# Kernel optimization log

Hardware: AMD Instinct MI355X
Metric: run time of the kernel (lower is better)

The kernel has to match this reference:

```python
import jax, jax.numpy as jnp
import numpy as np

N = 50_000       # nodes
E = 1_600_000    # edges per edge set (avg degree 32)
D = 128          # hidden dim
F_IN = 1273      # fixed num_features in NetGIN
G = 512          # graphs in batch
STEPS = 6        # Set2Set processing steps
BN_EPS = 1e-5


def setup_inputs() -> dict:
    key = jax.random.key(0)
    ks = iter(jax.random.split(key, 40))
    def rn(shape, fan_in):
        return jax.random.normal(next(ks), shape, jnp.float32) / np.float32(np.sqrt(fan_in))
    inp = {}
    inp["x"] = jax.random.normal(next(ks), (N, F_IN), jnp.float32)
    for i in (1, 2, 3):
        inp[f"edge_index_{i}"] = jax.random.randint(next(ks), (2, E), 0, N, jnp.int32)
    inp["batch"] = jnp.sort(jax.random.randint(next(ks), (N,), 0, G, jnp.int32))
    # GINConv MLPs: layer 1 has input F_IN, layers 2-6 have input D
    inp["conv1_W1"] = rn((3, F_IN, D), F_IN)
    inp["conv1_b1"] = jnp.zeros((3, D), jnp.float32)
    inp["conv_rest_W1"] = rn((5, 3, D, D), D)
    inp["conv_rest_b1"] = jnp.zeros((5, 3, D), jnp.float32)
    inp["conv_W2"] = rn((6, 3, D, D), D)
    inp["conv_b2"] = jnp.zeros((6, 3, D), jnp.float32)
    inp["conv_bn1_g"] = jnp.ones((6, 3, D), jnp.float32)
    inp["conv_bn1_b"] = jnp.zeros((6, 3, D), jnp.float32)
    inp["conv_bn2_g"] = jnp.ones((6, 3, D), jnp.float32)
    inp["conv_bn2_b"] = jnp.zeros((6, 3, D), jnp.float32)
    inp["conv_eps"] = jnp.zeros((6, 3), jnp.float32)  # train_eps=True, init 0
    # fusion MLPs (3*D -> D -> D)
    inp["mlp_W1"] = rn((6, 3 * D, D), 3 * D)
    inp["mlp_b1"] = jnp.zeros((6, D), jnp.float32)
    inp["mlp_bn1_g"] = jnp.ones((6, D), jnp.float32)
    inp["mlp_bn1_b"] = jnp.zeros((6, D), jnp.float32)
    inp["mlp_W2"] = rn((6, D, D), D)
    inp["mlp_b2"] = jnp.zeros((6, D), jnp.float32)
    inp["mlp_bn2_g"] = jnp.ones((6, D), jnp.float32)
    inp["mlp_bn2_b"] = jnp.zeros((6, D), jnp.float32)
    # Set2Set single-layer LSTM: input 2D, hidden D; gate order i,f,g,o
    inp["lstm_Wih"] = rn((4 * D, 2 * D), 2 * D)
    inp["lstm_Whh"] = rn((4 * D, D), D)
    inp["lstm_bih"] = jnp.zeros((4 * D,), jnp.float32)
    inp["lstm_bhh"] = jnp.zeros((4 * D,), jnp.float32)
    inp["fc1_W"] = rn((2 * D, D), 2 * D)
    inp["fc1_b"] = jnp.zeros((D,), jnp.float32)
    inp["fc4_W"] = rn((D, 12), D)
    inp["fc4_b"] = jnp.zeros((12,), jnp.float32)
    return inp


def _bn(x, g, b):
    # BatchNorm1d in training mode: batch statistics (biased var), eps=1e-5
    mu = jnp.mean(x, axis=0)
    var = jnp.var(x, axis=0)
    return g * (x - mu) * jax.lax.rsqrt(var + BN_EPS) + b


def _mlp2(h, W1, b1, g1, bb1, W2, b2, g2, bb2):
    h = jax.nn.relu(_bn(h @ W1 + b1, g1, bb1))
    return jax.nn.relu(_bn(h @ W2 + b2, g2, bb2))


def _gin(h, ei, eps, W1, b1, g1, bb1, W2, b2, g2, bb2):
    # sum-aggregate neighbor features: out[dst] += h[src]
    agg = jax.ops.segment_sum(h[ei[0]], ei[1], num_segments=h.shape[0])
    return _mlp2((1.0 + eps) * h + agg, W1, b1, g1, bb1, W2, b2, g2, bb2)


def _forward(x, conv1_W1, conv1_b1, conv_rest_W1, conv_rest_b1, conv_W2, conv_b2,
             conv_bn1_g, conv_bn1_b, conv_bn2_g, conv_bn2_b, conv_eps,
             mlp_W1, mlp_b1, mlp_bn1_g, mlp_bn1_b, mlp_W2, mlp_b2, mlp_bn2_g, mlp_bn2_b,
             lstm_Wih, lstm_Whh, lstm_bih, lstm_bhh, fc1_W, fc1_b, fc4_W, fc4_b,
             edge_index_1, edge_index_2, edge_index_3, batch):
    edges = (edge_index_1, edge_index_2, edge_index_3)
    h = x
    for l in range(6):
        xs = []
        for k in range(3):
            W1 = conv1_W1[k] if l == 0 else conv_rest_W1[l - 1, k]
            b1 = conv1_b1[k] if l == 0 else conv_rest_b1[l - 1, k]
            xk = jax.nn.relu(_gin(h, edges[k], conv_eps[l, k], W1, b1,
                                  conv_bn1_g[l, k], conv_bn1_b[l, k],
                                  conv_W2[l, k], conv_b2[l, k],
                                  conv_bn2_g[l, k], conv_bn2_b[l, k]))
            xs.append(xk)
        h = _mlp2(jnp.concatenate(xs, axis=-1),
                  mlp_W1[l], mlp_b1[l], mlp_bn1_g[l], mlp_bn1_b[l],
                  mlp_W2[l], mlp_b2[l], mlp_bn2_g[l], mlp_bn2_b[l])
    # Set2Set readout (processing_steps=6)
    q_star = jnp.zeros((G, 2 * D), h.dtype)
    hh = jnp.zeros((G, D), h.dtype)
    cc = jnp.zeros((G, D), h.dtype)
    for _ in range(STEPS):
        gates = q_star @ lstm_Wih.T + hh @ lstm_Whh.T + lstm_bih + lstm_bhh
        i_g, f_g, g_g, o_g = jnp.split(gates, 4, axis=-1)
        cc = jax.nn.sigmoid(f_g) * cc + jax.nn.sigmoid(i_g) * jnp.tanh(g_g)
        hh = jax.nn.sigmoid(o_g) * jnp.tanh(cc)
        q = hh
        e = jnp.sum(h * q[batch], axis=-1)              # [N]
        emax = jax.ops.segment_max(e, batch, num_segments=G)
        ex = jnp.exp(e - emax[batch])
        denom = jax.ops.segment_sum(ex, batch, num_segments=G)
        a = ex / denom[batch]                            # per-graph softmax
        r = jax.ops.segment_sum(a[:, None] * h, batch, num_segments=G)
        q_star = jnp.concatenate([q, r], axis=-1)
    out = jax.nn.relu(q_star @ fc1_W + fc1_b)
    return out @ fc4_W + fc4_b                           # [G, 12]


def reference(x, conv1_W1, conv1_b1, conv_rest_W1, conv_rest_b1, conv_W2, conv_b2,
              conv_bn1_g, conv_bn1_b, conv_bn2_g, conv_bn2_b, conv_eps,
              mlp_W1, mlp_b1, mlp_bn1_g, mlp_bn1_b, mlp_W2, mlp_b2, mlp_bn2_g, mlp_bn2_b,
              lstm_Wih, lstm_Whh, lstm_bih, lstm_bhh, fc1_W, fc1_b, fc4_W, fc4_b,
              edge_index_1, edge_index_2, edge_index_3, batch):
    return _forward(x, conv1_W1, conv1_b1, conv_rest_W1, conv_rest_b1, conv_W2, conv_b2,
                    conv_bn1_g, conv_bn1_b, conv_bn2_g, conv_bn2_b, conv_eps,
                    mlp_W1, mlp_b1, mlp_bn1_g, mlp_bn1_b, mlp_W2, mlp_b2, mlp_bn2_g, mlp_bn2_b,
                    lstm_Wih, lstm_Whh, lstm_bih, lstm_bhh, fc1_W, fc1_b, fc4_W, fc4_b,
                    edge_index_1, edge_index_2, edge_index_3, batch)
```

## Files before the change

kernel.cpp:

```cpp
#include <hip/hip_runtime.h>
#include <cstdint>
#include <cstddef>

#define NN 50000
#define EE 1600000
#define GG 512
#define FIN 1273

typedef unsigned short u16;
typedef unsigned int u32;
typedef __attribute__((ext_vector_type(8))) short short8;
typedef __attribute__((ext_vector_type(4))) float f32x4;

__device__ __forceinline__ float sigmf(float x) { return 1.f / (1.f + expf(-x)); }

__device__ __forceinline__ void splitbf(float v, u16& hi, u16& lo) {
    const u32 u = __float_as_uint(v);
    hi = (u16)(u >> 16);
    const float rem = v - __uint_as_float(u & 0xffff0000u);
    lo = (u16)(__float_as_uint(rem) >> 16);
}

__device__ __forceinline__ void gload_lds16(const void* g, void* l) {
    __builtin_amdgcn_global_load_lds(
        (const __attribute__((address_space(1))) void*)g,
        (__attribute__((address_space(3))) void*)l, 16, 0, 0);
}

template <int MODE>
__global__ __launch_bounds__(256) void gemm_bn(
    const float* __restrict__ A, size_t strideA, int lda, int K, int Kreal,
    const float* __restrict__ st, int stSlice, int stMat,
    const float* __restrict__ ga, const float* __restrict__ be,
    int gbSlice, int gbMat,
    const u16* __restrict__ Bhi, const u16* __restrict__ Blo, size_t strideB,
    const float* __restrict__ bias, int biasMat,
    float* __restrict__ C, int ldc, int coffStep,
    int M, int do_stats, float* __restrict__ stats_out, int ostatMat)
{
    __shared__ u16 lsAhi[128 * 64];
    __shared__ u16 lsAlo[128 * 64];
    __shared__ u16 lsBhi[128 * 64];
    __shared__ u16 lsBlo[128 * 64];
    const int tid = threadIdx.x;
    const int wave = tid >> 6, lane = tid & 63;
    const int mat = blockIdx.x;
    const int row0 = blockIdx.y * 128;
    const int coff = mat * coffStep;
    A += (size_t)mat * strideA;
    if (MODE == 1) {
        st += mat * stMat; ga += mat * gbMat; be += mat * gbMat;
    }
    if (bias) bias += mat * biasMat;
    if (do_stats) stats_out += mat * ostatMat;
    const u16* Bh = Bhi + (size_t)mat * strideB;
    const u16* Bl = Blo + (size_t)mat * strideB;
    const int wm = wave >> 1, wn = wave & 1;
    f32x4 acc[4][4] = {};

    for (int k0 = 0; k0 < K; k0 += 64) {
        if (k0) __syncthreads();
        float scv[8], shv[8];
        if (MODE == 1) {
            const int kb = k0 + (tid & 7) * 8;
            const int s = kb >> 7, d0 = kb & 127;
            const float* stS = st + s * stSlice;
            const float* gS  = ga + s * gbSlice;
            const float* beS = be + s * gbSlice;
            #pragma unroll
            for (int e = 0; e < 8; ++e) {
                const int d = d0 + e;
                const float mu = stS[d] * (1.f / NN);
                const float var = fmaxf(stS[128 + d] * (1.f / NN) - mu * mu, 0.f);
                const float sc = gS[d] * rsqrtf(var + 1e-5f);
                scv[e] = sc;
                shv[e] = beS[d] - sc * mu;
            }
        }
        #pragma unroll
        for (int i = 0; i < 4; ++i) {
            const int slot = i * 256 + tid;
            const int r = slot >> 3, ch = tid & 7;
            int gr = row0 + r; if (gr >= M) gr = M - 1;
            const int kb = k0 + ch * 8;
            u16 th[8], tl[8];
            if (MODE == 0) {
                const float* src = A + (size_t)gr * lda + kb;
                if (kb + 8 <= Kreal) {
                    const float4 v0 = *(const float4*)(src);
                    const float4 v1 = *(const float4*)(src + 4);
                    const float va[8] = {v0.x, v0.y, v0.z, v0.w,
                                         v1.x, v1.y, v1.z, v1.w};
                    #pragma unroll
                    for (int e = 0; e < 8; ++e) splitbf(va[e], th[e], tl[e]);
                } else {
                    #pragma unroll
                    for (int e = 0; e < 8; ++e) {
                        const float v = (kb + e < Kreal) ? src[e] : 0.f;
                        splitbf(v, th[e], tl[e]);
                    }
                }
            } else {
                const float* src = A + (size_t)gr * lda + kb;
                const float4 v0 = *(const float4*)(src);
                const float4 v1 = *(const float4*)(src + 4);
                const float va[8] = {v0.x, v0.y, v0.z, v0.w, v1.x, v1.y, v1.z, v1.w};
                #pragma unroll
                for (int e = 0; e < 8; ++e) {
                    const float y = fmaxf(fmaf(scv[e], va[e], shv[e]), 0.f);
                    splitbf(y, th[e], tl[e]);
                }
            }
            const int off = (r << 6) + ((ch ^ (r & 7)) << 3);
            *(short8*)&lsAhi[off] = *(const short8*)th;
            *(short8*)&lsAlo[off] = *(const short8*)tl;
        }
        #pragma unroll
        for (int i = 0; i < 4; ++i) {
            const int slot = i * 256 + wave * 64 + lane;
            const int r = slot >> 3, ch = slot & 7;
            const int sch = ch ^ (r & 7);
            const size_t goff = (size_t)r * K + k0 + sch * 8;
            const int lbase = (i * 256 + wave * 64) * 8;
            gload_lds16(Bh + goff, &lsBhi[lbase]);
            gload_lds16(Bl + goff, &lsBlo[lbase]);
        }
        __syncthreads();
        #pragma unroll
        for (int ks = 0; ks < 2; ++ks) {
            short8 ah[4], al[4], bh[4], bl[4];
            const int kch = ks * 4 + (lane >> 4);
            #pragma unroll
            for (int m = 0; m < 4; ++m) {
                const int r = wm * 64 + m * 16 + (lane & 15);
                const int off = (r << 6) + ((kch ^ (r & 7)) << 3);
                ah[m] = *(const short8*)&lsAhi[off];
                al[m] = *(const short8*)&lsAlo[off];
            }
            #pragma unroll
            for (int n = 0; n < 4; ++n) {
                const int c = wn * 64 + n * 16 + (lane & 15);
                const int off = (c << 6) + ((kch ^ (c & 7)) << 3);
                bh[n] = *(const short8*)&lsBhi[off];
                bl[n] = *(const short8*)&lsBlo[off];
            }
            #pragma unroll
            for (int m = 0; m < 4; ++m)
                #pragma unroll
                for (int n = 0; n < 4; ++n) {
                    acc[m][n] = __builtin_amdgcn_mfma_f32_16x16x32_bf16(
                        ah[m], bh[n], acc[m][n], 0, 0, 0);
                    acc[m][n] = __builtin_amdgcn_mfma_f32_16x16x32_bf16(
                        ah[m], bl[n], acc[m][n], 0, 0, 0);
                    acc[m][n] = __builtin_amdgcn_mfma_f32_16x16x32_bf16(
                        al[m], bh[n], acc[m][n], 0, 0, 0);
                }
        }
    }

    float colsum[4] = {0.f, 0.f, 0.f, 0.f}, colsq[4] = {0.f, 0.f, 0.f, 0.f};
    #pragma unroll
    for (int n = 0; n < 4; ++n) {
        const int c = wn * 64 + n * 16 + (lane & 15);
        const float bv = bias ? bias[c] : 0.f;
        #pragma unroll
        for (int m = 0; m < 4; ++m) {
            #pragma unroll
            for (int j = 0; j < 4; ++j) {
                const int gr = row0 + wm * 64 + m * 16 + ((lane >> 4) << 2) + j;
                if (gr < M) {
                    const float v = acc[m][n][j] + bv;
                    C[(size_t)gr * ldc + coff + c] = v;
                    colsum[n] += v; colsq[n] += v * v;
                }
            }
        }
    }
    if (do_stats) {
        float* ssum = (float*)lsBhi;
        float* ssq  = ssum + 128;
        __syncthreads();
        if (tid < 128) { ssum[tid] = 0.f; ssq[tid] = 0.f; }
        __syncthreads();
        #pragma unroll
        for (int n = 0; n < 4; ++n) {
            const int c = wn * 64 + n * 16 + (lane & 15);
            atomicAdd(&ssum[c], colsum[n]);
            atomicAdd(&ssq[c], colsq[n]);
        }
        __syncthreads();
        if (tid < 128) {
            atomicAdd(&stats_out[tid],       ssum[tid]);
            atomicAdd(&stats_out[128 + tid], ssq[tid]);
        }
    }
}

__global__ __launch_bounds__(256) void wt_cast2(const float* __restrict__ W,
                                                u16* __restrict__ Whi,
                                                u16* __restrict__ Wlo,
                                                int total, int K, int Kpad) {
    const int idx = blockIdx.x * 256 + threadIdx.x;
    if (idx >= total) return;
    const int perm = 128 * Kpad;
    const int m = idx / perm, rem = idx - m * perm;
    const int n = rem / Kpad, k = rem - n * Kpad;
    const float v = (k < K) ? W[(size_t)m * K * 128 + (size_t)k * 128 + n] : 0.f;
    u16 hi, lo;
    splitbf(v, hi, lo);
    Whi[idx] = hi; Wlo[idx] = lo;
}

template <bool BT>
__global__ __launch_bounds__(256) void gemm_f32(
    const float* __restrict__ A, const float* __restrict__ B,
    const float* __restrict__ bias, float* __restrict__ C,
    int M, int K, int Nc)
{
    __shared__ float As[32][68];
    __shared__ float Bs[32][132];
    const int tid = threadIdx.x;
    const int tx = tid & 15, ty = tid >> 4;
    const int row0 = blockIdx.x * 64, col0 = blockIdx.y * 128;
    float acc[4][8] = {};
    for (int k0 = 0; k0 < K; k0 += 32) {
        {
            const int kk = tid & 31, rb = tid >> 5;
            #pragma unroll
            for (int i = 0; i < 8; ++i) {
                const int r = rb + i * 8, gr = row0 + r, gk = k0 + kk;
                As[kk][r] = (gr < M && gk < K) ? A[(size_t)gr * K + gk] : 0.f;
            }
        }
        if (!BT) {
            const int c = tid & 127, kb = tid >> 7;
            #pragma unroll
            for (int i = 0; i < 16; ++i) {
                const int kk = kb + i * 2, gk = k0 + kk;
                Bs[kk][c] = (gk < K) ? B[(size_t)gk * Nc + col0 + c] : 0.f;
            }
        } else {
            const int kk = tid & 31, cb = tid >> 5;
            #pragma unroll
            for (int i = 0; i < 16; ++i) {
                const int c = cb + i * 8, gk = k0 + kk;
                Bs[kk][c] = (gk < K) ? B[(size_t)(col0 + c) * K + gk] : 0.f;
            }
        }
        __syncthreads();
        #pragma unroll 8
        for (int kk = 0; kk < 32; ++kk) {
            const float4 av  = *(const float4*)&As[kk][ty * 4];
            const float4 bv0 = *(const float4*)&Bs[kk][tx * 8];
            const float4 bv1 = *(const float4*)&Bs[kk][tx * 8 + 4];
            const float a[4] = {av.x, av.y, av.z, av.w};
            const float b[8] = {bv0.x, bv0.y, bv0.z, bv0.w, bv1.x, bv1.y, bv1.z, bv1.w};
            #pragma unroll
            for (int i = 0; i < 4; ++i)
                #pragma unroll
                for (int j = 0; j < 8; ++j)
                    acc[i][j] = fmaf(a[i], b[j], acc[i][j]);
        }
        __syncthreads();
    }
    #pragma unroll
    for (int j = 0; j < 8; ++j) {
        const float bv = bias ? bias[col0 + tx * 8 + j] : 0.f;
        #pragma unroll
        for (int i = 0; i < 4; ++i) acc[i][j] += bv;
    }
    #pragma unroll
    for (int i = 0; i < 4; ++i) {
        const int gr = row0 + ty * 4 + i;
        if (gr < M) {
            *(float4*)&C[(size_t)gr * Nc + col0 + tx * 8] =
                make_float4(acc[i][0], acc[i][1], acc[i][2], acc[i][3]);
            *(float4*)&C[(size_t)gr * Nc + col0 + tx * 8 + 4] =
                make_float4(acc[i][4], acc[i][5], acc[i][6], acc[i][7]);
        }
    }
}

__global__ __launch_bounds__(256) void count_deg(const int* __restrict__ dst,
                                                 int* __restrict__ deg) {
    const int e = blockIdx.x * 256 + threadIdx.x;
    if (e < EE) atomicAdd(&deg[dst[e]], 1);
}

__global__ __launch_bounds__(512) void scan1(const int* __restrict__ deg,
                                             int* __restrict__ scanned,
                                             int* __restrict__ bsum) {
    __shared__ int s[512];
    const int t = threadIdx.x;
    const int i = blockIdx.x * 512 + t;
    const int v = (i < NN) ? deg[i] : 0;
    s[t] = v; __syncthreads();
    for (int o = 1; o < 512; o <<= 1) {
        const int tv = (t >= o) ? s[t - o] : 0;
        __syncthreads();
        s[t] += tv;
        __syncthreads();
    }
    if (i < NN) scanned[i] = s[t];
    if (t == 511) bsum[blockIdx.x] = s[511];
}

__global__ __launch_bounds__(128) void scan2(int* __restrict__ bsum, int nb) {
    __shared__ int s[128];
    const int t = threadIdx.x;
    const int v = (t < nb) ? bsum[t] : 0;
    s[t] = v; __syncthreads();
    for (int o = 1; o < 128; o <<= 1) {
        const int tv = (t >= o) ? s[t - o] : 0;
        __syncthreads();
        s[t] += tv;
        __syncthreads();
    }
    if (t < nb) bsum[t] = s[t] - v;
}

__global__ __launch_bounds__(256) void scan3(const int* __restrict__ deg,
                                             const int* __restrict__ scanned,
                                             const int* __restrict__ bsum,
                                             int* __restrict__ rowptr,
                                             int* __restrict__ cursor) {
    const int i = blockIdx.x * 256 + threadIdx.x;
    if (i < NN) {
        const int v = bsum[i >> 9] + scanned[i] - deg[i];
        rowptr[i] = v; cursor[i] = v;
    }
    if (i == 0) rowptr[NN] = EE;
}

__global__ __launch_bounds__(256) void fill_csr(const int* __restrict__ src,
                                                const int* __restrict__ dst,
                                                int* __restrict__ cursor,
                                                int* __restrict__ csrc) {
    const int e = blockIdx.x * 256 + threadIdx.x;
    if (e < EE) {
        const int pos = atomicAdd(&cursor[dst[e]], 1);
        csrc[pos] = src[e];
    }
}

__global__ __launch_bounds__(256) void agg_combine(
    const float* __restrict__ X, int ldp4, int colOff4,
    const int* __restrict__ rowptr, const int* __restrict__ csrc,
    const float* __restrict__ b1,
    const float* __restrict__ eps_arr, int eps_idx,
    float* __restrict__ z, float* __restrict__ stats)
{
    __shared__ float red[256];
    const int tid = threadIdx.x, lane = tid & 63, wave = tid >> 6;
    const float e1 = 1.f + eps_arr[eps_idx];
    const int half = lane >> 5;
    const int l32 = lane & 31;
    const float4* p4 = (const float4*)X + colOff4;
    float s[4] = {0.f, 0.f, 0.f, 0.f}, q[4] = {0.f, 0.f, 0.f, 0.f};
    float4 bv = make_float4(0.f, 0.f, 0.f, 0.f);
    if (lane < 32) bv = ((const float4*)b1)[l32];
    red[tid] = 0.f;
    __syncthreads();
    const int nbase = blockIdx.x * 16 + wave * 4;
    for (int t = 0; t < 4; ++t) {
        const int wid = nbase + t;
        const int s0 = rowptr[wid], s1 = rowptr[wid + 1];
        float ax = 0.f, ay = 0.f, az = 0.f, aw = 0.f;
        int j = s0;
        for (; j + 15 < s1; j += 16) {
            const int r0 = csrc[j + half],      r1 = csrc[j + 2 + half];
            const int r2 = csrc[j + 4 + half],  r3 = csrc[j + 6 + half];
            const int r4 = csrc[j + 8 + half],  r5 = csrc[j + 10 + half];
            const int r6 = csrc[j + 12 + half], r7 = csrc[j + 14 + half];
            const float4 v0 = p4[(size_t)r0 * ldp4 + l32];
            const float4 v1 = p4[(size_t)r1 * ldp4 + l32];
            const float4 v2 = p4[(size_t)r2 * ldp4 + l32];
            const float4 v3 = p4[(size_t)r3 * ldp4 + l32];
            const float4 v4 = p4[(size_t)r4 * ldp4 + l32];
            const float4 v5 = p4[(size_t)r5 * ldp4 + l32];
            const float4 v6 = p4[(size_t)r6 * ldp4 + l32];
            const float4 v7 = p4[(size_t)r7 * ldp4 + l32];
            ax += (v0.x + v1.x) + (v2.x + v3.x) + (v4.x + v5.x) + (v6.x + v7.x);
            ay += (v0.y + v1.y) + (v2.y + v3.y) + (v4.y + v5.y) + (v6.y + v7.y);
            az += (v0.z + v1.z) + (v2.z + v3.z) + (v4.z + v5.z) + (v6.z + v7.z);
            aw += (v0.w + v1.w) + (v2.w + v3.w) + (v4.w + v5.w) + (v6.w + v7.w);
        }
        for (; j + 7 < s1; j += 8) {
            const int r0 = csrc[j + half],     r1 = csrc[j + 2 + half];
            const int r2 = csrc[j + 4 + half], r3 = csrc[j + 6 + half];
            const float4 v0 = p4[(size_t)r0 * ldp4 + l32];
            const float4 v1 = p4[(size_t)r1 * ldp4 + l32];
            const float4 v2 = p4[(size_t)r2 * ldp4 + l32];
            const float4 v3 = p4[(size_t)r3 * ldp4 + l32];
            ax += (v0.x + v1.x) + (v2.x + v3.x);
            ay += (v0.y + v1.y) + (v2.y + v3.y);
            az += (v0.z + v1.z) + (v2.z + v3.z);
            aw += (v0.w + v1.w) + (v2.w + v3.w);
        }
        for (; j + 3 < s1; j += 4) {
            const int ra = csrc[j + half];
            const int rb = csrc[j + 2 + half];
            const float4 v0 = p4[(size_t)ra * ldp4 + l32];
            const float4 v1 = p4[(size_t)rb * ldp4 + l32];
            ax += v0.x + v1.x; ay += v0.y + v1.y;
            az += v0.z + v1.z; aw += v0.w + v1.w;
        }
        for (; j + 1 < s1; j += 2) {
            const int ra = csrc[j + half];
            const float4 v0 = p4[(size_t)ra * ldp4 + l32];
            ax += v0.x; ay += v0.y; az += v0.z; aw += v0.w;
        }
        if (j < s1 && half == 0) {
            const float4 v0 = p4[(size_t)csrc[j] * ldp4 + l32];
            ax += v0.x; ay += v0.y; az += v0.z; aw += v0.w;
        }
        ax += __shfl_down(ax, 32, 64);
        ay += __shfl_down(ay, 32, 64);
        az += __shfl_down(az, 32, 64);
        aw += __shfl_down(aw, 32, 64);
        if (lane < 32) {
            const float4 self = p4[(size_t)wid * ldp4 + l32];
            float4 zv;
            zv.x = fmaf(e1, self.x, ax + bv.x);
            zv.y = fmaf(e1, self.y, ay + bv.y);
            zv.z = fmaf(e1, self.z, az + bv.z);
            zv.w = fmaf(e1, self.w, aw + bv.w);
            ((float4*)z)[(size_t)wid * 32 + l32] = zv;
            s[0] += zv.x; s[1] += zv.y; s[2] += zv.z; s[3] += zv.w;
            q[0] += zv.x * zv.x; q[1] += zv.y * zv.y;
            q[2] += zv.z * zv.z; q[3] += zv.w * zv.w;
        }
    }
    if (lane < 32) {
        const int d = l32 * 4;
        #pragma unroll
        for (int c = 0; c < 4; ++c) {
            atomicAdd(&red[d + c], s[c]);
            atomicAdd(&red[128 + d + c], q[c]);
        }
    }
    __syncthreads();
    atomicAdd(&stats[tid], red[tid]);
}

__global__ __launch_bounds__(256) void bn_relu_f32(
    const float* __restrict__ xin, const float* __restrict__ stats,
    const float* __restrict__ gamma, const float* __restrict__ beta,
    float* __restrict__ out)
{
    const size_t i = (size_t)blockIdx.x * 256 + threadIdx.x;
    if (i >= (size_t)NN * 64) return;
    const int d = (int)(i & 63) * 2;
    const float inv_n = 1.f / NN;
    const float mu0 = stats[d] * inv_n,     mu1 = stats[d + 1] * inv_n;
    const float v0 = fmaxf(stats[128 + d] * inv_n - mu0 * mu0, 0.f);
    const float v1 = fmaxf(stats[129 + d] * inv_n - mu1 * mu1, 0.f);
    const float s0 = gamma[d] * rsqrtf(v0 + 1e-5f);
    const float s1 = gamma[d + 1] * rsqrtf(v1 + 1e-5f);
    const float2 xv = ((const float2*)xin)[i];
    const float y0 = fmaxf(fmaf(s0, xv.x - mu0, beta[d]), 0.f);
    const float y1 = fmaxf(fmaf(s1, xv.y - mu1, beta[d + 1]), 0.f);
    ((float2*)out)[i] = make_float2(y0, y1);
}

__global__ __launch_bounds__(256) void seg_starts(const int* __restrict__ batch,
                                                  int* __restrict__ gstart) {
    const int i = blockIdx.x * 256 + threadIdx.x;
    if (i >= NN) return;
    const int b = batch[i];
    if (i == 0) { for (int g = 0; g <= b; ++g) gstart[g] = 0; }
    else {
        const int pb = batch[i - 1];
        for (int g = pb + 1; g <= b; ++g) gstart[g] = i;
    }
    if (i == NN - 1) { for (int g = b + 1; g <= GG; ++g) gstart[g] = NN; }
}

__global__ __launch_bounds__(256) void pack_wcat(const float* __restrict__ Wih,
                                                 const float* __restrict__ Whh,
                                                 float* __restrict__ Wcat) {
    const int i = blockIdx.x * 256 + threadIdx.x;
    if (i >= 512 * 384) return;
    const int j = i / 384, k = i - j * 384;
    Wcat[i] = (k < 256) ? Wih[j * 256 + k] : Whh[j * 128 + (k - 256)];
}

__global__ __launch_bounds__(256) void lstm_kernel(
    const float* __restrict__ gates, const float* __restrict__ bih,
    const float* __restrict__ bhh, float* __restrict__ cc, float* __restrict__ S)
{
    const int i = blockIdx.x * 256 + threadIdx.x;
    if (i >= GG * 128) return;
    const int g = i >> 7, d = i & 127;
    const float* gr = gates + (size_t)g * 512;
    const float ig = gr[d]       + bih[d]       + bhh[d];
    const float fg = gr[128 + d] + bih[128 + d] + bhh[128 + d];
    const float gv = gr[256 + d] + bih[256 + d] + bhh[256 + d];
    const float og = gr[384 + d] + bih[384 + d] + bhh[384 + d];
    const float c  = sigmf(fg) * cc[i] + sigmf(ig) * tanhf(gv);
    const float hv = sigmf(og) * tanhf(c);
    cc[i] = c;
    S[(size_t)g * 384 + d] = hv;
    S[(size_t)g * 384 + 256 + d] = hv;
}

__global__ __launch_bounds__(256) void attend_kernel(
    const float* __restrict__ h, float* __restrict__ S,
    float* __restrict__ ews, const int* __restrict__ gstart)
{
    const int g = blockIdx.x;
    const int rs = gstart[g], re = gstart[g + 1];
    const int tid = threadIdx.x, lane = tid & 63, w = tid >> 6;
    __shared__ float q[128];
    __shared__ float red[8];
    if (tid < 128) q[tid] = S[(size_t)g * 384 + 256 + tid];
    __syncthreads();
    const float2* h2 = (const float2*)h;
    float lmax = -1e30f;
    for (int n = rs + w; n < re; n += 4) {
        const float2 hv = h2[(size_t)n * 64 + lane];
        float p = hv.x * q[2 * lane] + hv.y * q[2 * lane + 1];
        #pragma unroll
        for (int o = 32; o; o >>= 1) p += __shfl_down(p, o, 64);
        if (lane == 0) { ews[n] = p; lmax = fmaxf(lmax, p); }
    }
    if (lane == 0) red[w] = lmax;
    __syncthreads();
    const float m = fmaxf(fmaxf(red[0], red[1]), fmaxf(red[2], red[3]));
    __syncthreads();
    float lsum = 0.f;
    for (int n = rs + tid; n < re; n += 256) {
        const float ex = expf(ews[n] - m);
        ews[n] = ex; lsum += ex;
    }
    #pragma unroll
    for (int o = 32; o; o >>= 1) lsum += __shfl_down(lsum, o, 64);
    if (lane == 0) red[w] = lsum;
    __syncthreads();
    const float denom = red[0] + red[1] + red[2] + red[3];
    if (tid < 128) {
        float acc = 0.f;
        for (int n = rs; n < re; ++n)
            acc = fmaf(ews[n], h[(size_t)n * 128 + tid], acc);
        S[(size_t)g * 384 + 128 + tid] = (denom > 0.f) ? acc / denom : 0.f;
    }
}

__global__ __launch_bounds__(128) void fc1_kernel(const float* __restrict__ S,
                                                  const float* __restrict__ W,
                                                  const float* __restrict__ b,
                                                  float* __restrict__ out1) {
    const int g = blockIdx.x, d = threadIdx.x;
    __shared__ float qs[256];
    qs[d] = S[(size_t)g * 384 + d];
    qs[128 + d] = S[(size_t)g * 384 + 128 + d];
    __syncthreads();
    float acc = b[d];
    for (int k = 0; k < 256; ++k) acc = fmaf(qs[k], W[k * 128 + d], acc);
    out1[(size_t)g * 128 + d] = fmaxf(acc, 0.f);
}

__global__ __launch_bounds__(256) void fc4_kernel(const float* __restrict__ out1,
                                                  const float* __restrict__ W,
                                                  const float* __restrict__ b,
                                                  float* __restrict__ out) {
    const int i = blockIdx.x * 256 + threadIdx.x;
    if (i >= GG * 12) return;
    const int g = i / 12, j = i - g * 12;
    float acc = b[j];
    for (int d = 0; d < 128; ++d)
        acc = fmaf(out1[(size_t)g * 128 + d], W[d * 12 + j], acc);
    out[i] = acc;
}

extern "C" void kernel_launch(void* const* d_in, const int* in_sizes, int n_in,
                              void* d_out, int out_size, void* d_ws, size_t ws_size,
                              hipStream_t stream)
{
    const float* x        = (const float*)d_in[0];
    const int*   eidx[3]  = {(const int*)d_in[1], (const int*)d_in[2], (const int*)d_in[3]};
    const int*   batch    = (const int*)d_in[4];
    const float* conv1_W1     = (const float*)d_in[5];
    const float* conv1_b1     = (const float*)d_in[6];
    const float* conv_rest_W1 = (const float*)d_in[7];
    const float* conv_rest_b1 = (const float*)d_in[8];
    const float* conv_W2      = (const float*)d_in[9];
    const float* conv_b2      = (const float*)d_in[10];
    const float* conv_bn1_g   = (const float*)d_in[11];
    const float* conv_bn1_b   = (const float*)d_in[12];
    const float* conv_bn2_g   = (const float*)d_in[13];
    const float* conv_bn2_b   = (const float*)d_in[14];
    const float* conv_eps     = (const float*)d_in[15];
    const float* mlp_W1       = (const float*)d_in[16];
    const float* mlp_b1       = (const float*)d_in[17];
    const float* mlp_bn1_g    = (const float*)d_in[18];
    const float* mlp_bn1_b    = (const float*)d_in[19];
    const float* mlp_W2       = (const float*)d_in[20];
    const float* mlp_b2       = (const float*)d_in[21];
    const float* mlp_bn2_g    = (const float*)d_in[22];
    const float* mlp_bn2_b    = (const float*)d_in[23];
    const float* lstm_Wih     = (const float*)d_in[24];
    const float* lstm_Whh     = (const float*)d_in[25];
    const float* lstm_bih     = (const float*)d_in[26];
    const float* lstm_bhh     = (const float*)d_in[27];
    const float* fc1_W        = (const float*)d_in[28];
    const float* fc1_b        = (const float*)d_in[29];
    const float* fc4_W        = (const float*)d_in[30];
    const float* fc4_b        = (const float*)d_in[31];
    float* outp = (float*)d_out;

    float* f = (float*)d_ws;
    size_t fo = 0;
    float* X     = f + fo; fo += (size_t)NN * 384;
    float* zs    = f + fo; fo += (size_t)NN * 384;
    float* zm2   = f + fo; fo += (size_t)NN * 128;
    float* ews   = f + fo; fo += NN;
    float* stats = f + fo; fo += 48 * 256;
    float* S     = f + fo; fo += (size_t)GG * 384;
    float* ccb   = f + fo; fo += (size_t)GG * 128;
    float* gates = f + fo; fo += (size_t)GG * 512;
    float* Wcat  = f + fo; fo += (size_t)512 * 384;
    float* hbuf = X;
    fo = (fo + 7) & ~(size_t)7;
    u16* b = (u16*)(f + fo);
    size_t bo = 0;
    u16* c1_hi   = b + bo; bo += (size_t)3 * 128 * 1280;
    u16* c1_lo   = b + bo; bo += (size_t)3 * 128 * 1280;
    u16* rw1_hi  = b + bo; bo += (size_t)15 * 128 * 128;
    u16* rw1_lo  = b + bo; bo += (size_t)15 * 128 * 128;
    u16* w2_hi   = b + bo; bo += (size_t)18 * 128 * 128;
    u16* w2_lo   = b + bo; bo += (size_t)18 * 128 * 128;
    u16* mw1_hi  = b + bo; bo += (size_t)6 * 128 * 384;
    u16* mw1_lo  = b + bo; bo += (size_t)6 * 128 * 384;
    u16* mw2_hi  = b + bo; bo += (size_t)6 * 128 * 128;
    u16* mw2_lo  = b + bo; bo += (size_t)6 * 128 * 128;
    int* ip = (int*)(b + bo);
    size_t io = 0;
    int* rowptr[3]; int* csrc[3];
    for (int s = 0; s < 3; ++s) { rowptr[s] = ip + io; io += NN + 1; }
    for (int s = 0; s < 3; ++s) { csrc[s]   = ip + io; io += EE; }
    int* deg     = ip + io; io += NN;
    int* cursor  = ip + io; io += NN;
    int* scanned = ip + io; io += NN;
    int* bsum    = ip + io; io += 128;
    int* gstart  = ip + io; io += GG + 1;
    const size_t need = fo * 4 + bo * 2 + io * 4;
    if (ws_size < need) return;

    const int NBLK_SCAN = (NN + 511) / 512;

    {
        int t;
        t = 3 * 128 * 1280;
        wt_cast2<<<(t + 255) / 256, 256, 0, stream>>>(conv1_W1, c1_hi, c1_lo, t, FIN, 1280);
        t = 15 * 128 * 128;
        wt_cast2<<<(t + 255) / 256, 256, 0, stream>>>(conv_rest_W1, rw1_hi, rw1_lo, t, 128, 128);
        t = 18 * 128 * 128;
        wt_cast2<<<(t + 255) / 256, 256, 0, stream>>>(conv_W2, w2_hi, w2_lo, t, 128, 128);
        t = 6 * 128 * 384;
        wt_cast2<<<(t + 255) / 256, 256, 0, stream>>>(mlp_W1, mw1_hi, mw1_lo, t, 384, 384);
        t = 6 * 128 * 128;
        wt_cast2<<<(t + 255) / 256, 256, 0, stream>>>(mlp_W2, mw2_hi, mw2_lo, t, 128, 128);
    }

    for (int s = 0; s < 3; ++s) {
        hipMemsetAsync(deg, 0, NN * sizeof(int), stream);
        count_deg<<<(EE + 255) / 256, 256, 0, stream>>>(eidx[s] + EE, deg);
        scan1<<<NBLK_SCAN, 512, 0, stream>>>(deg, scanned, bsum);
        scan2<<<1, 128, 0, stream>>>(bsum, NBLK_SCAN);
        scan3<<<(NN + 255) / 256, 256, 0, stream>>>(deg, scanned, bsum, rowptr[s], cursor);
        fill_csr<<<(EE + 255) / 256, 256, 0, stream>>>(eidx[s], eidx[s] + EE, cursor, csrc[s]);
    }
    seg_starts<<<(NN + 255) / 256, 256, 0, stream>>>(batch, gstart);
    hipMemsetAsync(stats, 0, 48 * 256 * sizeof(float), stream);
    hipMemsetAsync(S, 0, (size_t)GG * 384 * sizeof(float), stream);
    hipMemsetAsync(ccb, 0, (size_t)GG * 128 * sizeof(float), stream);

    const int G128 = (NN + 127) / 128;
    const int AGG_GRID = NN / 16;

    for (int l = 0; l < 6; ++l) {
        float* stL    = stats + (size_t)l * 8 * 256;
        float* slotF1 = stL + 6 * 256;
        float* slotF2 = stL + 7 * 256;

        if (l == 0)
            gemm_bn<0><<<dim3(3, G128), 256, 0, stream>>>(
                x, 0, FIN, 1280, FIN,
                nullptr, 0, 0, nullptr, nullptr, 0, 0,
                c1_hi, c1_lo, (size_t)128 * 1280,
                nullptr, 0, X, 384, 128, NN, 0, nullptr, 0);
        else
            gemm_bn<1><<<dim3(3, G128), 256, 0, stream>>>(
                zm2, 0, 128, 128, 128,
                stats + (size_t)((l - 1) * 8 + 7) * 256, 0, 0,
                mlp_bn2_g + (l - 1) * 128, mlp_bn2_b + (l - 1) * 128, 0, 0,
                rw1_hi + (size_t)(l - 1) * 3 * 128 * 128,
                rw1_lo + (size_t)(l - 1) * 3 * 128 * 128, (size_t)128 * 128,
                nullptr, 0, X, 384, 128, NN, 0, nullptr, 0);

        for (int k = 0; k < 3; ++k) {
            const int lk = l * 3 + k;
            const float* b1 = (l == 0) ? conv1_b1 + k * 128
                                       : conv_rest_b1 + ((l - 1) * 3 + k) * 128;
            agg_combine<<<AGG_GRID, 256, 0, stream>>>(
                X, 96, k * 32, rowptr[k], csrc[k], b1, conv_eps, lk,
                zs + (size_t)k * NN * 128, stL + (size_t)k * 512);
        }

        gemm_bn<1><<<dim3(3, G128), 256, 0, stream>>>(
            zs, (size_t)NN * 128, 128, 128, 128,
            stL, 0, 512,
            conv_bn1_g + l * 3 * 128, conv_bn1_b + l * 3 * 128, 0, 128,
            w2_hi + (size_t)l * 3 * 128 * 128,
            w2_lo + (size_t)l * 3 * 128 * 128, (size_t)128 * 128,
            conv_b2 + l * 3 * 128, 128,
            X, 384, 128, NN, 1, stL + 256, 512);

        gemm_bn<1><<<dim3(1, G128), 256, 0, stream>>>(
            X, 0, 384, 384, 384,
            stL + 256, 512, 0,
            conv_bn2_g + l * 3 * 128, conv_bn2_b + l * 3 * 128, 128, 0,
            mw1_hi + (size_t)l * 128 * 384, mw1_lo + (size_t)l * 128 * 384, 0,
            mlp_b1 + l * 128, 0, zs, 128, 0, NN, 1, slotF1, 0);

        gemm_bn<1><<<dim3(1, G128), 256, 0, stream>>>(
            zs, 0, 128, 128, 128,
            slotF1, 0, 0,
            mlp_bn1_g + l * 128, mlp_bn1_b + l * 128, 0, 0,
            mw2_hi + (size_t)l * 128 * 128, mw2_lo + (size_t)l * 128 * 128, 0,
            mlp_b2 + l * 128, 0, zm2, 128, 0, NN, 1, slotF2, 0);
    }
    bn_relu_f32<<<(NN * 64 + 255) / 256, 256, 0, stream>>>(
        zm2, stats + (size_t)(5 * 8 + 7) * 256,
        mlp_bn2_g + 5 * 128, mlp_bn2_b + 5 * 128, hbuf);

    pack_wcat<<<(512 * 384 + 255) / 256, 256, 0, stream>>>(lstm_Wih, lstm_Whh, Wcat);
    for (int t = 0; t < 6; ++t) {
        gemm_f32<true><<<dim3(8, 4), 256, 0, stream>>>(
            S, Wcat, nullptr, gates, GG, 384, 512);
        lstm_kernel<<<(GG * 128 + 255) / 256, 256, 0, stream>>>(
            gates, lstm_bih, lstm_bhh, ccb, S);
        attend_kernel<<<GG, 256, 0, stream>>>(hbuf, S, ews, gstart);
    }
    fc1_kernel<<<GG, 128, 0, stream>>>(S, fc1_W, fc1_b, gates);
    fc4_kernel<<<(GG * 12 + 255) / 256, 256, 0, stream>>>(gates, fc4_W, fc4_b, outp);
}
```

Baseline: 5.298 ms.

## Load GEMM A operands directly to registers and remap blocks across matrices

Splits the templated GEMM into a layer-0 kernel and a direct-load kernel. The direct kernel skips the LDS staging for the A operand, applying BN+ReLU and the bf16 hi/lo split in registers straight from global memory, and keeps only B in LDS. Both kernels remap a 1-D grid so consecutive blocks cover the three weight matrices for neighbouring row tiles, which is meant to improve cache reuse of the shared A rows. The three agg_combine launches are merged into one launch with a y-dimension. The cost is redundant global A loads and redundant BN-parameter computation per wave, traded for half the LDS use and possibly higher occupancy.

```diff
diff --git a/kernel.cpp b/kernel.cpp
--- a/kernel.cpp
+++ b/kernel.cpp
@@ -27,32 +27,28 @@
         (__attribute__((address_space(3))) void*)l, 16, 0, 0);
 }
 
-template <int MODE>
-__global__ __launch_bounds__(256) void gemm_bn(
-    const float* __restrict__ A, size_t strideA, int lda, int K, int Kreal,
-    const float* __restrict__ st, int stSlice, int stMat,
-    const float* __restrict__ ga, const float* __restrict__ be,
-    int gbSlice, int gbMat,
+__device__ __forceinline__ bool remap3(int f, int nRow, int& mat, int& rt) {
+    const int g = f / 24, w = f - g * 24;
+    rt = g * 8 + (w & 7);
+    mat = w >> 3;
+    return rt < nRow;
+}
+
+__global__ __launch_bounds__(256) void gemm_l0(
+    const float* __restrict__ A, int lda, int K, int Kreal,
     const u16* __restrict__ Bhi, const u16* __restrict__ Blo, size_t strideB,
-    const float* __restrict__ bias, int biasMat,
-    float* __restrict__ C, int ldc, int coffStep,
-    int M, int do_stats, float* __restrict__ stats_out, int ostatMat)
+    float* __restrict__ C, int ldc, int coffStep, int M, int nRow)
 {
     __shared__ u16 lsAhi[128 * 64];
     __shared__ u16 lsAlo[128 * 64];
     __shared__ u16 lsBhi[128 * 64];
     __shared__ u16 lsBlo[128 * 64];
+    int mat, rt;
+    if (!remap3(blockIdx.x, nRow, mat, rt)) return;
     const int tid = threadIdx.x;
     const int wave = tid >> 6, lane = tid & 63;
-    const int mat = blockIdx.x;
-    const int row0 = blockIdx.y * 128;
+    const int row0 = rt * 128;
     const int coff = mat * coffStep;
-    A += (size_t)mat * strideA;
-    if (MODE == 1) {
-        st += mat * stMat; ga += mat * gbMat; be += mat * gbMat;
-    }
-    if (bias) bias += mat * biasMat;
-    if (do_stats) stats_out += mat * ostatMat;
     const u16* Bh = Bhi + (size_t)mat * strideB;
     const u16* Bl = Blo + (size_t)mat * strideB;
     const int wm = wave >> 1, wn = wave & 1;
@@ -60,23 +56,6 @@
 
     for (int k0 = 0; k0 < K; k0 += 64) {
         if (k0) __syncthreads();
-        float scv[8], shv[8];
-        if (MODE == 1) {
-            const int kb = k0 + (tid & 7) * 8;
-            const int s = kb >> 7, d0 = kb & 127;
-            const float* stS = st + s * stSlice;
-            const float* gS  = ga + s * gbSlice;
-            const float* beS = be + s * gbSlice;
-            #pragma unroll
-            for (int e = 0; e < 8; ++e) {
-                const int d = d0 + e;
-                const float mu = stS[d] * (1.f / NN);
-                const float var = fmaxf(stS[128 + d] * (1.f / NN) - mu * mu, 0.f);
-                const float sc = gS[d] * rsqrtf(var + 1e-5f);
-                scv[e] = sc;
-                shv[e] = beS[d] - sc * mu;
-            }
-        }
         #pragma unroll
         for (int i = 0; i < 4; ++i) {
             const int slot = i * 256 + tid;
@@ -84,31 +63,19 @@
             int gr = row0 + r; if (gr >= M) gr = M - 1;
             const int kb = k0 + ch * 8;
             u16 th[8], tl[8];
-            if (MODE == 0) {
-                const float* src = A + (size_t)gr * lda + kb;
-                if (kb + 8 <= Kreal) {
-                    const float4 v0 = *(const float4*)(src);
-                    const float4 v1 = *(const float4*)(src + 4);
-                    const float va[8] = {v0.x, v0.y, v0.z, v0.w,
-                                         v1.x, v1.y, v1.z, v1.w};
-                    #pragma unroll
-                    for (int e = 0; e < 8; ++e) splitbf(va[e], th[e], tl[e]);
-                } else {
-                    #pragma unroll
-                    for (int e = 0; e < 8; ++e) {
-                        const float v = (kb + e < Kreal) ? src[e] : 0.f;
-                        splitbf(v, th[e], tl[e]);
-                    }
-                }
-            } else {
-                const float* src = A + (size_t)gr * lda + kb;
+            const float* src = A + (size_t)gr * lda + kb;
+            if (kb + 8 <= Kreal) {
                 const float4 v0 = *(const float4*)(src);
                 const float4 v1 = *(const float4*)(src + 4);
-                const float va[8] = {v0.x, v0.y, v0.z, v0.w, v1.x, v1.y, v1.z, v1.w};
+                const float va[8] = {v0.x, v0.y, v0.z, v0.w,
+                                     v1.x, v1.y, v1.z, v1.w};
+                #pragma unroll
+                for (int e = 0; e < 8; ++e) splitbf(va[e], th[e], tl[e]);
+            } else {
                 #pragma unroll
                 for (int e = 0; e < 8; ++e) {
-                    const float y = fmaxf(fmaf(scv[e], va[e], shv[e]), 0.f);
-                    splitbf(y, th[e], tl[e]);
+                    const float v = (kb + e < Kreal) ? src[e] : 0.f;
+                    splitbf(v, th[e], tl[e]);
                 }
             }
             const int off = (r << 6) + ((ch ^ (r & 7)) << 3);
@@ -155,6 +122,127 @@
                     acc[m][n] = __builtin_amdgcn_mfma_f32_16x16x32_bf16(
                         al[m], bh[n], acc[m][n], 0, 0, 0);
                 }
+        }
+    }
+    #pragma unroll
+    for (int n = 0; n < 4; ++n) {
+        const int c = wn * 64 + n * 16 + (lane & 15);
+        #pragma unroll
+        for (int m = 0; m < 4; ++m) {
+            #pragma unroll
+            for (int j = 0; j < 4; ++j) {
+                const int gr = row0 + wm * 64 + m * 16 + ((lane >> 4) << 2) + j;
+                if (gr < M)
+                    C[(size_t)gr * ldc + coff + c] = acc[m][n][j];
+            }
+        }
+    }
+}
+
+__global__ __launch_bounds__(256) void gemm_dir(
+    const float* __restrict__ A, size_t strideA, int lda, int K,
+    const float* __restrict__ st, int stSlice, int stMat,
+    const float* __restrict__ ga, const float* __restrict__ be,
+    int gbSlice, int gbMat,
+    const u16* __restrict__ Bhi, const u16* __restrict__ Blo, size_t strideB,
+    const float* __restrict__ bias, int biasMat,
+    float* __restrict__ C, int ldc, int coffStep,
+    int M, int do_stats, float* __restrict__ stats_out, int ostatMat,
+    int nMat, int nRow)
+{
+    __shared__ u16 lsBhi[128 * 64];
+    __shared__ u16 lsBlo[128 * 64];
+    int mat, rt;
+    if (nMat == 3) {
+        if (!remap3(blockIdx.x, nRow, mat, rt)) return;
+    } else { mat = 0; rt = blockIdx.x; }
+    const int tid = threadIdx.x;
+    const int wave = tid >> 6, lane = tid & 63;
+    const int row0 = rt * 128;
+    const int wm = wave >> 1, wn = wave & 1;
+    A += (size_t)mat * strideA;
+    st += mat * stMat; ga += mat * gbMat; be += mat * gbMat;
+    if (bias) bias += mat * biasMat;
+    if (do_stats) stats_out += mat * ostatMat;
+    const u16* Bh = Bhi + (size_t)mat * strideB;
+    const u16* Bl = Blo + (size_t)mat * strideB;
+    const int coff = mat * coffStep;
+    f32x4 acc[4][4] = {};
+
+    int arow[4];
+    #pragma unroll
+    for (int m = 0; m < 4; ++m) {
+        int r = row0 + wm * 64 + m * 16 + (lane & 15);
+        if (r >= M) r = M - 1;
+        arow[m] = r;
+    }
+
+    for (int k0 = 0; k0 < K; k0 += 64) {
+        if (k0) __syncthreads();
+        #pragma unroll
+        for (int i = 0; i < 4; ++i) {
+            const int slot = i * 256 + wave * 64 + lane;
+            const int r = slot >> 3, ch = slot & 7;
+            const int sch = ch ^ (r & 7);
+            const size_t goff = (size_t)r * K + k0 + sch * 8;
+            const int lbase = (i * 256 + wave * 64) * 8;
+            gload_lds16(Bh + goff, &lsBhi[lbase]);
+            gload_lds16(Bl + goff, &lsBlo[lbase]);
+        }
+        __syncthreads();
+        #pragma unroll
+        for (int ks = 0; ks < 2; ++ks) {
+            const int kch = ks * 4 + (lane >> 4);
+            const int kb = k0 + kch * 8;
+            float scv[8], shv[8];
+            {
+                const int s = kb >> 7, d0 = kb & 127;
+                const float* stS = st + s * stSlice;
+                const float* gS  = ga + s * gbSlice;
+                const float* beS = be + s * gbSlice;
+                #pragma unroll
+                for (int e = 0; e < 8; ++e) {
+                    const int d = d0 + e;
+                    const float mu = stS[d] * (1.f / NN);
+                    const float var = fmaxf(stS[128 + d] * (1.f / NN) - mu * mu, 0.f);
+                    const float sc = gS[d] * rsqrtf(var + 1e-5f);
+                    scv[e] = sc;
+                    shv[e] = beS[d] - sc * mu;
+                }
+            }
+            short8 ah[4], al[4];
+            #pragma unroll
+            for (int m = 0; m < 4; ++m) {
+                const float* src = A + (size_t)arow[m] * lda + kb;
+                const float4 v0 = *(const float4*)(src);
+                const float4 v1 = *(const float4*)(src + 4);
+                const float va[8] = {v0.x, v0.y, v0.z, v0.w,
+                                     v1.x, v1.y, v1.z, v1.w};
+                u16 th[8], tl[8];
+                #pragma unroll
+                for (int e = 0; e < 8; ++e) {
+                    const float y = fmaxf(fmaf(scv[e], va[e], shv[e]), 0.f);
+                    splitbf(y, th[e], tl[e]);
+                }
+                ah[m] = *(const short8*)th;
+                al[m] = *(const short8*)tl;
+            }
+            #pragma unroll
+            for (int n = 0; n < 4; ++n) {
+                const int c = wn * 64 + n * 16 + (lane & 15);
+                const int off = (c << 6) + ((kch ^ (c & 7)) << 3);
+                const short8 bh = *(const short8*)&lsBhi[off];
+                const short8 bl = *(const short8*)&lsBlo[off];
+                #pragma unroll
+                for (int m = 0; m < 4; ++m) {
+                    acc[m][n] = __builtin_amdgcn_mfma_f32_16x16x32_bf16(
+                        ah[m], bh, acc[m][n], 0, 0, 0);
+                    acc[m][n] = __builtin_amdgcn_mfma_f32_16x16x32_bf16(
+                        ah[m], bl, acc[m][n], 0, 0, 0);
+                    acc[m][n] = __builtin_amdgcn_mfma_f32_16x16x32_bf16(
+                        al[m], bh, acc[m][n], 0, 0, 0);
+                }
+            }
         }
     }
 
@@ -344,18 +432,24 @@
 }
 
 __global__ __launch_bounds__(256) void agg_combine(
-    const float* __restrict__ X, int ldp4, int colOff4,
-    const int* __restrict__ rowptr, const int* __restrict__ csrc,
-    const float* __restrict__ b1,
-    const float* __restrict__ eps_arr, int eps_idx,
-    float* __restrict__ z, float* __restrict__ stats)
+    const float* __restrict__ X, int ldp4,
+    const int* __restrict__ rowptrB, const int* __restrict__ csrcB,
+    const float* __restrict__ b1B,
+    const float* __restrict__ eps_arr, int epsBase,
+    float* __restrict__ zB, float* __restrict__ statsB)
 {
     __shared__ float red[256];
+    const int k = blockIdx.y;
+    const int* rowptr = rowptrB + (size_t)k * (NN + 1);
+    const int* csrc   = csrcB + (size_t)k * EE;
+    const float* b1   = b1B + k * 128;
+    float* z          = zB + (size_t)k * NN * 128;
+    float* stats      = statsB + (size_t)k * 512;
     const int tid = threadIdx.x, lane = tid & 63, wave = tid >> 6;
-    const float e1 = 1.f + eps_arr[eps_idx];
+    const float e1 = 1.f + eps_arr[epsBase + k];
     const int half = lane >> 5;
     const int l32 = lane & 31;
-    const float4* p4 = (const float4*)X + colOff4;
+    const float4* p4 = (const float4*)X + k * 32;
     float s[4] = {0.f, 0.f, 0.f, 0.f}, q[4] = {0.f, 0.f, 0.f, 0.f};
     float4 bv = make_float4(0.f, 0.f, 0.f, 0.f);
     if (lane < 32) bv = ((const float4*)b1)[l32];
@@ -636,9 +730,8 @@
     u16* mw2_lo  = b + bo; bo += (size_t)6 * 128 * 128;
     int* ip = (int*)(b + bo);
     size_t io = 0;
-    int* rowptr[3]; int* csrc[3];
-    for (int s = 0; s < 3; ++s) { rowptr[s] = ip + io; io += NN + 1; }
-    for (int s = 0; s < 3; ++s) { csrc[s]   = ip + io; io += EE; }
+    int* rowptr0 = ip + io; io += (size_t)3 * (NN + 1);
+    int* csrc0   = ip + io; io += (size_t)3 * EE;
     int* deg     = ip + io; io += NN;
     int* cursor  = ip + io; io += NN;
     int* scanned = ip + io; io += NN;
@@ -664,12 +757,14 @@
     }
 
     for (int s = 0; s < 3; ++s) {
+        int* rowptr = rowptr0 + (size_t)s * (NN + 1);
+        int* csrc   = csrc0 + (size_t)s * EE;
         hipMemsetAsync(deg, 0, NN * sizeof(int), stream);
         count_deg<<<(EE + 255) / 256, 256, 0, stream>>>(eidx[s] + EE, deg);
         scan1<<<NBLK_SCAN, 512, 0, stream>>>(deg, scanned, bsum);
         scan2<<<1, 128, 0, stream>>>(bsum, NBLK_SCAN);
-        scan3<<<(NN + 255) / 256, 256, 0, stream>>>(deg, scanned, bsum, rowptr[s], cursor);
-        fill_csr<<<(EE + 255) / 256, 256, 0, stream>>>(eidx[s], eidx[s] + EE, cursor, csrc[s]);
+        scan3<<<(NN + 255) / 256, 256, 0, stream>>>(deg, scanned, bsum, rowptr, cursor);
+        fill_csr<<<(EE + 255) / 256, 256, 0, stream>>>(eidx[s], eidx[s] + EE, cursor, csrc);
     }
     seg_starts<<<(NN + 255) / 256, 256, 0, stream>>>(batch, gstart);
     hipMemsetAsync(stats, 0, 48 * 256 * sizeof(float), stream);
@@ -677,6 +772,7 @@
     hipMemsetAsync(ccb, 0, (size_t)GG * 128 * sizeof(float), stream);
 
     const int G128 = (NN + 127) / 128;
+    const int G3   = 24 * ((G128 + 7) / 8);
     const int AGG_GRID = NN / 16;
 
     for (int l = 0; l < 6; ++l) {
@@ -685,51 +781,46 @@
         float* slotF2 = stL + 7 * 256;
 
         if (l == 0)
-            gemm_bn<0><<<dim3(3, G128), 256, 0, stream>>>(
-                x, 0, FIN, 1280, FIN,
-                nullptr, 0, 0, nullptr, nullptr, 0, 0,
-                c1_hi, c1_lo, (size_t)128 * 1280,
-                nullptr, 0, X, 384, 128, NN, 0, nullptr, 0);
+            gemm_l0<<<G3, 256, 0, stream>>>(
+                x, FIN, 1280, FIN, c1_hi, c1_lo, (size_t)128 * 1280,
+                X, 384, 128, NN, G128);
         else
-            gemm_bn<1><<<dim3(3, G128), 256, 0, stream>>>(
-                zm2, 0, 128, 128, 128,
+            gemm_dir<<<G3, 256, 0, stream>>>(
+                zm2, 0, 128, 128,
                 stats + (size_t)((l - 1) * 8 + 7) * 256, 0, 0,
                 mlp_bn2_g + (l - 1) * 128, mlp_bn2_b + (l - 1) * 128, 0, 0,
                 rw1_hi + (size_t)(l - 1) * 3 * 128 * 128,
                 rw1_lo + (size_t)(l - 1) * 3 * 128 * 128, (size_t)128 * 128,
-                nullptr, 0, X, 384, 128, NN, 0, nullptr, 0);
-
-        for (int k = 0; k < 3; ++k) {
-            const int lk = l * 3 + k;
-            const float* b1 = (l == 0) ? conv1_b1 + k * 128
-                                       : conv_rest_b1 + ((l - 1) * 3 + k) * 128;
-            agg_combine<<<AGG_GRID, 256, 0, stream>>>(
-                X, 96, k * 32, rowptr[k], csrc[k], b1, conv_eps, lk,
-                zs + (size_t)k * NN * 128, stL + (size_t)k * 512);
-        }
-
-        gemm_bn<1><<<dim3(3, G128), 256, 0, stream>>>(
-            zs, (size_t)NN * 128, 128, 128, 128,
+                nullptr, 0, X, 384, 128, NN, 0, nullptr, 0, 3, G128);
+
+        {
+            const float* b1B = (l == 0) ? conv1_b1 : conv_rest_b1 + (l - 1) * 3 * 128;
+            agg_combine<<<dim3(AGG_GRID, 3), 256, 0, stream>>>(
+                X, 96, rowptr0, csrc0, b1B, conv_eps, l * 3, zs, stL);
+        }
+
+        gemm_dir<<<G3, 256, 0, stream>>>(
+            zs, (size_t)NN * 128, 128, 128,
             stL, 0, 512,
             conv_bn1_g + l * 3 * 128, conv_bn1_b + l * 3 * 128, 0, 128,
             w2_hi + (size_t)l * 3 * 128 * 128,
             w2_lo + (size_t)l * 3 * 128 * 128, (size_t)128 * 128,
             conv_b2 + l * 3 * 128, 128,
-            X, 384, 128, NN, 1, stL + 256, 512);
-
-        gemm_bn<1><<<dim3(1, G128), 256, 0, stream>>>(
-            X, 0, 384, 384, 384,
+            X, 384, 128, NN, 1, stL + 256, 512, 3, G128);
+
+        gemm_dir<<<G128, 256, 0, stream>>>(
+            X, 0, 384, 384,
             stL + 256, 512, 0,
             conv_bn2_g + l * 3 * 128, conv_bn2_b + l * 3 * 128, 128, 0,
             mw1_hi + (size_t)l * 128 * 384, mw1_lo + (size_t)l * 128 * 384, 0,
-            mlp_b1 + l * 128, 0, zs, 128, 0, NN, 1, slotF1, 0);
-
-        gemm_bn<1><<<dim3(1, G128), 256, 0, stream>>>(
-            zs, 0, 128, 128, 128,
+            mlp_b1 + l * 128, 0, zs, 128, 0, NN, 1, slotF1, 0, 1, G128);
+
+        gemm_dir<<<G128, 256, 0, stream>>>(
+            zs, 0, 128, 128,
             slotF1, 0, 0,
             mlp_bn1_g + l * 128, mlp_bn1_b + l * 128, 0, 0,
             mw2_hi + (size_t)l * 128 * 128, mw2_lo + (size_t)l * 128 * 128, 0,
-            mlp_b2 + l * 128, 0, zm2, 128, 0, NN, 1, slotF2, 0);
+            mlp_b2 + l * 128, 0, zm2, 128, 0, NN, 1, slotF2, 0, 1, G128);
     }
     bn_relu_f32<<<(NN * 64 + 255) / 256, 256, 0, stream>>>(
         zm2, stats + (size_t)(5 * 8 + 7) * 256,
```

Measured after the change: 5.202 ms. About the same (-1.8%).
